# Performance work log

Measured on AMD Instinct MI355X. Metric: run time of the kernel, lower is better.

Reference implementation:

```python
import jax, jax.numpy as jnp
import numpy as np

TEMPERATURE = 0.07


def setup_inputs() -> dict:
    key = jax.random.key(0)
    k1, k2, k3 = jax.random.split(key, 3)
    B, D = 8192, 256
    projections = jax.random.normal(k1, (B, D), dtype=jnp.float32)
    affordance_ids = jax.random.randint(k2, (B,), 0, 16, dtype=jnp.int64)
    instance_ids = jax.random.randint(k3, (B,), 0, 4096, dtype=jnp.int64)
    return {
        "projections": projections,
        "affordance_ids": affordance_ids,
        "instance_ids": instance_ids,
    }


def reference(projections, affordance_ids, instance_ids):
    B = projections.shape[0]
    # (B, B) similarity logits
    sim = jnp.matmul(projections, projections.T) / TEMPERATURE
    aff_mask = affordance_ids[:, None] == affordance_ids[None, :]
    inst_mask = instance_ids[:, None] == instance_ids[None, :]
    positive_mask = aff_mask & (~inst_mask)
    self_mask = jnp.eye(B, dtype=bool)
    # per-row logsumexp over all j != i (stable, single pass)
    masked_sim = jnp.where(self_mask, -jnp.inf, sim)
    lse = jax.nn.logsumexp(masked_sim, axis=1)  # (B,)
    # loss per positive pair: -sim[i,j] + lse[i]
    per_pair = jnp.where(positive_mask, lse[:, None] - sim, 0.0)
    num_pairs = jnp.sum(positive_mask)
    total = jnp.sum(per_pair)
    return jnp.where(num_pairs > 0, total / num_pairs.astype(sim.dtype), 0.0)
```

## Files before the change

kernel.cpp:

```cpp
#include <hip/hip_runtime.h>
#include <hip/hip_bf16.h>
#include <stdint.h>

#define BN 8192
#define DK 256
#define KLOG2E_T 20.609929155556617f
#define INV_T 14.285714285714286f
#define NEGINF (-3.0e38f)

typedef short vshort8 __attribute__((ext_vector_type(8)));
typedef float vfloat16 __attribute__((ext_vector_type(16)));

__device__ __forceinline__ void gload16(const void* g, void* lds) {
  __builtin_amdgcn_global_load_lds(
      (const __attribute__((address_space(1))) unsigned int*)g,
      (__attribute__((address_space(3))) unsigned int*)lds, 16, 0, 0);
}

__global__ __launch_bounds__(256) void prep_g(
    const float* __restrict__ P, const int* __restrict__ aff,
    const int* __restrict__ inst, ushort* __restrict__ Pb,
    int* __restrict__ keys, int* __restrict__ head, int* __restrict__ nxt,
    int* __restrict__ cntA, float* __restrict__ G) {
  __shared__ float4 Gl[4][16][64];
  __shared__ int hist[16];
  const int t = threadIdx.x;
  const int rg = t >> 6, c = t & 63;
  for (int idx = t; idx < 4096; idx += 256)
    ((float4*)Gl)[idx] = make_float4(0.f, 0.f, 0.f, 0.f);
  if (t < 16) hist[t] = 0;
  __syncthreads();
  const int r0 = blockIdx.x * 64;
  for (int k = 0; k < 16; ++k) {
    const int r = r0 + k * 4 + rg;
    float4 v = ((const float4*)(P + (size_t)r * DK))[c];
    ushort4 h;
    __hip_bfloat16 b;
    b = __float2bfloat16(v.x); h.x = __builtin_bit_cast(unsigned short, b);
    b = __float2bfloat16(v.y); h.y = __builtin_bit_cast(unsigned short, b);
    b = __float2bfloat16(v.z); h.z = __builtin_bit_cast(unsigned short, b);
    b = __float2bfloat16(v.w); h.w = __builtin_bit_cast(unsigned short, b);
    ((ushort4*)(Pb + (size_t)r * DK))[c] = h;
    const int a = aff[r];
    float4 g = Gl[rg][a][c];
    g.x += v.x; g.y += v.y; g.z += v.z; g.w += v.w;
    Gl[rg][a][c] = g;
  }
  if (t < 64) {
    const int g = r0 + t;
    const int a = aff[g];
    const int k = (a << 12) | inst[g];
    keys[g] = k;
    nxt[g] = atomicExch(&head[k], g + 1);
    atomicAdd(&hist[a], 1);
  }
  __syncthreads();
  if (t < 16) atomicAdd(&cntA[t], hist[t]);
  for (int idx = t; idx < 1024; idx += 256) {
    const int a = idx >> 6, cc = idx & 63;
    float4 s0 = Gl[0][a][cc], s1 = Gl[1][a][cc];
    float4 s2 = Gl[2][a][cc], s3 = Gl[3][a][cc];
    atomicAdd(&G[a * 256 + cc * 4 + 0], s0.x + s1.x + s2.x + s3.x);
    atomicAdd(&G[a * 256 + cc * 4 + 1], s0.y + s1.y + s2.y + s3.y);
    atomicAdd(&G[a * 256 + cc * 4 + 2], s0.z + s1.z + s2.z + s3.z);
    atomicAdd(&G[a * 256 + cc * 4 + 3], s0.w + s1.w + s2.w + s3.w);
  }
}

__global__ __launch_bounds__(512, 2) void fused_kernel(
    const ushort* __restrict__ Pb, float2* __restrict__ stats) {
  __shared__ __align__(16) char AbufB[8 * 128 * 64];
  __shared__ __align__(16) char BbufB[2 * 512 * 64];
  __shared__ float2 red[8][2][32];

  const int tid = threadIdx.x;
  const int w = tid >> 6;
  const int l = tid & 63;
  const int lo = l & 31;
  const int hi = l >> 5;
  const int iw = w >> 2;
  const int jw = w & 3;

  const int bid = blockIdx.x;
  const int xcd = bid & 7;
  const int local = bid >> 3;
  const int jc = (xcd << 1) | (local & 1);
  const int it = local >> 1;
  const int ibase = it * 128;
  const int jcbase = jc * 512;

  const int srow = tid >> 2;
  const int sswz = ((tid & 3) ^ ((srow >> 1) & 3)) * 16;
  const char* gA = (const char*)(Pb + (size_t)ibase * DK);
  const char* gB = (const char*)(Pb + (size_t)jcbase * DK);

#pragma unroll
  for (int e = 0; e < 8; ++e)
    gload16(gA + (size_t)srow * 512 + e * 64 + sswz, AbufB + e * 8192 + tid * 16);
#pragma unroll
  for (int e = 0; e < 4; ++e)
    gload16(gB + (size_t)(e * 128 + srow) * 512 + sswz,
            BbufB + e * 8192 + tid * 16);
  __syncthreads();

  const int rowa = iw * 64 + lo;
  const int rowb = jw * 128 + lo;
  const int rsw = (lo >> 1) & 3;
  const int sw0 = ((0 + hi) ^ rsw) * 16;
  const int sw1 = ((2 + hi) ^ rsw) * 16;

  vfloat16 acc[2][4];
#pragma unroll
  for (int mi = 0; mi < 2; ++mi)
#pragma unroll
    for (int nj = 0; nj < 4; ++nj)
#pragma unroll
      for (int r = 0; r < 16; ++r) acc[mi][nj][r] = 0.f;

  for (int kc = 0; kc < 8; ++kc) {
    if (kc < 7) {
      char* dst = BbufB + ((kc + 1) & 1) * 32768 + tid * 16;
      const char* src = gB + (size_t)srow * 512 + (kc + 1) * 64 + sswz;
#pragma unroll
      for (int e = 0; e < 4; ++e)
        gload16(src + (size_t)e * 128 * 512, dst + e * 8192);
    }
    const char* As = AbufB + kc * 8192;
    const char* Bs = BbufB + (kc & 1) * 32768;
#pragma unroll
    for (int kk = 0; kk < 2; ++kk) {
      const int so = kk ? sw1 : sw0;
      vshort8 a0 = *(const vshort8*)(As + rowa * 64 + so);
      vshort8 a1 = *(const vshort8*)(As + (rowa + 32) * 64 + so);
#pragma unroll
      for (int nj = 0; nj < 4; ++nj) {
        vshort8 jf = *(const vshort8*)(Bs + (rowb + nj * 32) * 64 + so);
        acc[0][nj] = __builtin_amdgcn_mfma_f32_32x32x16_bf16(jf, a0, acc[0][nj], 0, 0, 0);
        acc[1][nj] = __builtin_amdgcn_mfma_f32_32x32x16_bf16(jf, a1, acc[1][nj], 0, 0, 0);
      }
    }
    __syncthreads();
  }

  float mx[2] = {NEGINF, NEGINF};
#pragma unroll
  for (int mi = 0; mi < 2; ++mi) {
    const int gib = ibase + iw * 64 + mi * 32;
#pragma unroll
    for (int nj = 0; nj < 4; ++nj) {
      const bool dia = gib == (jcbase + jw * 128 + nj * 32);
      if (dia) {
#pragma unroll
        for (int r = 0; r < 16; ++r) {
          const int jj = (r & 3) + 8 * (r >> 2) + 4 * hi;
          if (jj == lo) acc[mi][nj][r] = NEGINF;
        }
      }
#pragma unroll
      for (int r = 0; r < 16; ++r) mx[mi] = fmaxf(mx[mi], acc[mi][nj][r]);
    }
  }
  mx[0] = fmaxf(mx[0], __shfl_xor(mx[0], 32));
  mx[1] = fmaxf(mx[1], __shfl_xor(mx[1], 32));
  float s[2] = {0.f, 0.f};
#pragma unroll
  for (int mi = 0; mi < 2; ++mi) {
    const float rc = -mx[mi] * KLOG2E_T;
#pragma unroll
    for (int nj = 0; nj < 4; ++nj)
#pragma unroll
      for (int r = 0; r < 16; ++r)
        s[mi] += exp2f(fmaf(acc[mi][nj][r], KLOG2E_T, rc));
  }
  s[0] += __shfl_xor(s[0], 32);
  s[1] += __shfl_xor(s[1], 32);
  if (l < 32) {
    red[w][0][lo] = make_float2(mx[0], s[0]);
    red[w][1][lo] = make_float2(mx[1], s[1]);
  }
  __syncthreads();
  if (tid < 128) {
    const int iw2 = tid >> 6, mi2 = (tid >> 5) & 1, lo2 = tid & 31;
    float2 a = red[iw2 * 4 + 0][mi2][lo2];
    float mm = a.x, ss = a.y;
#pragma unroll
    for (int j2 = 1; j2 < 4; ++j2) {
      float2 b = red[iw2 * 4 + j2][mi2][lo2];
      float M = fmaxf(mm, b.x);
      ss = ss * exp2f((mm - M) * KLOG2E_T) + b.y * exp2f((b.x - M) * KLOG2E_T);
      mm = M;
    }
    stats[(size_t)jc * BN + ibase + iw2 * 64 + mi2 * 32 + lo2] = make_float2(mm, ss);
  }
}

__global__ __launch_bounds__(256) void final_rows(
    const float2* __restrict__ stats, const float* __restrict__ P,
    const float* __restrict__ G, const int* __restrict__ keys,
    const int* __restrict__ head, const int* __restrict__ nxt,
    const int* __restrict__ cntA, float2* __restrict__ part) {
  const int t = threadIdx.x;
  const int rloc = t >> 6;
  const int lane = t & 63;
  const int i = blockIdx.x * 4 + rloc;

  float2 st = stats[(size_t)(lane & 15) * BN + i];
  float mm = st.x, ss = st.y;
#pragma unroll
  for (int off = 1; off < 16; off <<= 1) {
    float mo = __shfl_xor(mm, off);
    float so = __shfl_xor(ss, off);
    float M = fmaxf(mm, mo);
    ss = ss * exp2f((mm - M) * KLOG2E_T) + so * exp2f((mo - M) * KLOG2E_T);
    mm = M;
  }
  const float lse = logf(ss) + mm * INV_T;

  const int key = keys[i];
  const int a = key >> 12;
  float4 p4 = ((const float4*)(P + (size_t)i * 256))[lane];
  float4 g4 = ((const float4*)(G + a * 256))[lane];
  float acc = p4.x * g4.x + p4.y * g4.y + p4.z * g4.z + p4.w * g4.w;
  int cnt = 0;
  int j = head[key];
  while (j > 0) {
    const int jr = j - 1;
    float4 q4 = ((const float4*)(P + (size_t)jr * 256))[lane];
    acc -= p4.x * q4.x + p4.y * q4.y + p4.z * q4.z + p4.w * q4.w;
    cnt++;
    j = nxt[jr];
  }
#pragma unroll
  for (int off = 1; off < 64; off <<= 1) acc += __shfl_xor(acc, off);
  const float pc = (float)(cntA[a] - cnt);
  const float contrib = pc * lse - acc * INV_T;

  __shared__ float cs[4], ps[4];
  if (lane == 0) { cs[rloc] = contrib; ps[rloc] = pc; }
  __syncthreads();
  if (t == 0)
    part[blockIdx.x] = make_float2(cs[0] + cs[1] + cs[2] + cs[3],
                                   ps[0] + ps[1] + ps[2] + ps[3]);
}

__global__ void finalize(const float2* __restrict__ part, float* __restrict__ out) {
  const int t = threadIdx.x;
  float c = 0.f, p = 0.f;
  for (int k = t; k < 2048; k += 256) {
    float2 v = part[k];
    c += v.x;
    p += v.y;
  }
#pragma unroll
  for (int off = 1; off < 64; off <<= 1) {
    c += __shfl_xor(c, off);
    p += __shfl_xor(p, off);
  }
  __shared__ float cs[4], ps[4];
  if ((t & 63) == 0) { cs[t >> 6] = c; ps[t >> 6] = p; }
  __syncthreads();
  if (t == 0) {
    c = cs[0] + cs[1] + cs[2] + cs[3];
    p = ps[0] + ps[1] + ps[2] + ps[3];
    out[0] = (p > 0.f) ? (c / p) : 0.f;
  }
}

extern "C" void kernel_launch(void* const* d_in, const int* in_sizes, int n_in,
                              void* d_out, int out_size, void* d_ws, size_t ws_size,
                              hipStream_t stream) {
  const float* P = (const float*)d_in[0];
  const int* aff = (const int*)d_in[1];
  const int* inst = (const int*)d_in[2];
  char* ws = (char*)d_ws;
  ushort* Pb    = (ushort*)(ws);
  int*    keys  = (int*)(ws + 4194304);
  int*    nxt   = (int*)(ws + 4227072);
  int*    head  = (int*)(ws + 4259840);
  float*  G     = (float*)(ws + 4521984);
  int*    cntA  = (int*)(ws + 4538368);
  float2* stats = (float2*)(ws + 4538496);
  float2* part  = (float2*)(ws + 5587072);
  float* out = (float*)d_out;

  hipMemsetAsync(head, 0, 278592, stream);
  prep_g<<<128, 256, 0, stream>>>(P, aff, inst, Pb, keys, head, nxt, cntA, G);
  fused_kernel<<<1024, 512, 0, stream>>>(Pb, stats);
  final_rows<<<2048, 256, 0, stream>>>(stats, P, G, keys, head, nxt, cntA, part);
  finalize<<<1, 256, 0, stream>>>(part, out);
}
```

Before: 91.98 us.

## Retile fused Gram kernel to 256x256 blocks with 4-wave 128x128 warp tiles

The fused similarity kernel moves from a 128x512 block tile with 8 waves of 64x128 to a 256x256 block tile with 4 waves, each computing 128x128 (4x4 MFMA tiles). A and B are both streamed in 128-byte K slices with double buffering and an 8-way XOR swizzle, where before all of A was resident. The column-chunk count doubles to 32, so the stats buffer grows and final_rows merges 32 partial max/sum pairs per row. The aim is higher MFMA-to-LDS-read reuse per wave, at the cost of more accumulator registers (256 floats per lane), lower occupancy, and a deeper final merge.

Result: slower. 99.70 us (+8.4%).

```diff
diff --git a/kernel.cpp b/kernel.cpp
--- a/kernel.cpp
+++ b/kernel.cpp
@@ -67,131 +67,128 @@
   }
 }
 
-__global__ __launch_bounds__(512, 2) void fused_kernel(
+__global__ __launch_bounds__(256, 1) void fused_kernel(
     const ushort* __restrict__ Pb, float2* __restrict__ stats) {
-  __shared__ __align__(16) char AbufB[8 * 128 * 64];
-  __shared__ __align__(16) char BbufB[2 * 512 * 64];
-  __shared__ float2 red[8][2][32];
+  __shared__ __align__(16) char Ab[2][32768];
+  __shared__ __align__(16) char Bb[2][32768];
+  __shared__ float2 red[2][256];
 
   const int tid = threadIdx.x;
   const int w = tid >> 6;
   const int l = tid & 63;
   const int lo = l & 31;
   const int hi = l >> 5;
-  const int iw = w >> 2;
-  const int jw = w & 3;
+  const int iw = w >> 1;
+  const int jw = w & 1;
 
   const int bid = blockIdx.x;
   const int xcd = bid & 7;
-  const int local = bid >> 3;
-  const int jc = (xcd << 1) | (local & 1);
-  const int it = local >> 1;
-  const int ibase = it * 128;
-  const int jcbase = jc * 512;
-
-  const int srow = tid >> 2;
-  const int sswz = ((tid & 3) ^ ((srow >> 1) & 3)) * 16;
+  const int inner = (bid >> 3) & 3;
+  const int it = bid >> 5;
+  const int jc = xcd * 4 + inner;
+  const int ibase = it * 256;
+  const int jcbase = jc * 256;
+
+  const int trow = tid >> 3;
+  const int sswz = ((tid & 7) ^ (trow & 7)) * 16;
   const char* gA = (const char*)(Pb + (size_t)ibase * DK);
   const char* gB = (const char*)(Pb + (size_t)jcbase * DK);
 
-#pragma unroll
-  for (int e = 0; e < 8; ++e)
-    gload16(gA + (size_t)srow * 512 + e * 64 + sswz, AbufB + e * 8192 + tid * 16);
-#pragma unroll
-  for (int e = 0; e < 4; ++e)
-    gload16(gB + (size_t)(e * 128 + srow) * 512 + sswz,
-            BbufB + e * 8192 + tid * 16);
-  __syncthreads();
-
-  const int rowa = iw * 64 + lo;
-  const int rowb = jw * 128 + lo;
-  const int rsw = (lo >> 1) & 3;
-  const int sw0 = ((0 + hi) ^ rsw) * 16;
-  const int sw1 = ((2 + hi) ^ rsw) * 16;
-
-  vfloat16 acc[2][4];
-#pragma unroll
-  for (int mi = 0; mi < 2; ++mi)
+#define STAGE(ks, bsel)                                                        \
+  {                                                                            \
+    const int ko = (ks) * 128;                                                 \
+    _Pragma("unroll") for (int e = 0; e < 8; ++e) {                            \
+      gload16(gA + (size_t)(trow + 32 * e) * 512 + ko + sswz,                  \
+              Ab[bsel] + e * 4096 + tid * 16);                                 \
+      gload16(gB + (size_t)(trow + 32 * e) * 512 + ko + sswz,                  \
+              Bb[bsel] + e * 4096 + tid * 16);                                 \
+    }                                                                          \
+  }
+
+  STAGE(0, 0);
+
+  vfloat16 acc[4][4];
+#pragma unroll
+  for (int mi = 0; mi < 4; ++mi)
 #pragma unroll
     for (int nj = 0; nj < 4; ++nj)
 #pragma unroll
       for (int r = 0; r < 16; ++r) acc[mi][nj][r] = 0.f;
 
-  for (int kc = 0; kc < 8; ++kc) {
-    if (kc < 7) {
-      char* dst = BbufB + ((kc + 1) & 1) * 32768 + tid * 16;
-      const char* src = gB + (size_t)srow * 512 + (kc + 1) * 64 + sswz;
-#pragma unroll
-      for (int e = 0; e < 4; ++e)
-        gload16(src + (size_t)e * 128 * 512, dst + e * 8192);
-    }
-    const char* As = AbufB + kc * 8192;
-    const char* Bs = BbufB + (kc & 1) * 32768;
-#pragma unroll
-    for (int kk = 0; kk < 2; ++kk) {
-      const int so = kk ? sw1 : sw0;
-      vshort8 a0 = *(const vshort8*)(As + rowa * 64 + so);
-      vshort8 a1 = *(const vshort8*)(As + (rowa + 32) * 64 + so);
-#pragma unroll
-      for (int nj = 0; nj < 4; ++nj) {
-        vshort8 jf = *(const vshort8*)(Bs + (rowb + nj * 32) * 64 + so);
-        acc[0][nj] = __builtin_amdgcn_mfma_f32_32x32x16_bf16(jf, a0, acc[0][nj], 0, 0, 0);
-        acc[1][nj] = __builtin_amdgcn_mfma_f32_32x32x16_bf16(jf, a1, acc[1][nj], 0, 0, 0);
+  const int rAb = iw * 128 + lo;
+  const int rBb = jw * 128 + lo;
+
+  __syncthreads();
+
+  for (int ks = 0; ks < 4; ++ks) {
+    if (ks < 3) STAGE(ks + 1, (ks + 1) & 1);
+    const char* As = Ab[ks & 1];
+    const char* Bs = Bb[ks & 1];
+#pragma unroll
+    for (int kk = 0; kk < 4; ++kk) {
+      const int so = ((kk * 2 + hi) ^ (lo & 7)) * 16;
+      vshort8 af0 = *(const vshort8*)(As + (rAb + 0) * 128 + so);
+      vshort8 af1 = *(const vshort8*)(As + (rAb + 32) * 128 + so);
+      vshort8 af2 = *(const vshort8*)(As + (rAb + 64) * 128 + so);
+      vshort8 af3 = *(const vshort8*)(As + (rAb + 96) * 128 + so);
+      vshort8 bf0 = *(const vshort8*)(Bs + (rBb + 0) * 128 + so);
+      vshort8 bf1 = *(const vshort8*)(Bs + (rBb + 32) * 128 + so);
+      vshort8 bf2 = *(const vshort8*)(Bs + (rBb + 64) * 128 + so);
+      vshort8 bf3 = *(const vshort8*)(Bs + (rBb + 96) * 128 + so);
+#pragma unroll
+      for (int mi = 0; mi < 4; ++mi) {
+        vshort8 af = mi == 0 ? af0 : mi == 1 ? af1 : mi == 2 ? af2 : af3;
+        acc[mi][0] = __builtin_amdgcn_mfma_f32_32x32x16_bf16(bf0, af, acc[mi][0], 0, 0, 0);
+        acc[mi][1] = __builtin_amdgcn_mfma_f32_32x32x16_bf16(bf1, af, acc[mi][1], 0, 0, 0);
+        acc[mi][2] = __builtin_amdgcn_mfma_f32_32x32x16_bf16(bf2, af, acc[mi][2], 0, 0, 0);
+        acc[mi][3] = __builtin_amdgcn_mfma_f32_32x32x16_bf16(bf3, af, acc[mi][3], 0, 0, 0);
       }
     }
     __syncthreads();
   }
 
-  float mx[2] = {NEGINF, NEGINF};
-#pragma unroll
-  for (int mi = 0; mi < 2; ++mi) {
-    const int gib = ibase + iw * 64 + mi * 32;
+#pragma unroll
+  for (int mi = 0; mi < 4; ++mi) {
+    const int gib = ibase + iw * 128 + mi * 32;
 #pragma unroll
     for (int nj = 0; nj < 4; ++nj) {
-      const bool dia = gib == (jcbase + jw * 128 + nj * 32);
-      if (dia) {
+      if (gib == (jcbase + jw * 128 + nj * 32)) {
 #pragma unroll
         for (int r = 0; r < 16; ++r) {
           const int jj = (r & 3) + 8 * (r >> 2) + 4 * hi;
           if (jj == lo) acc[mi][nj][r] = NEGINF;
         }
       }
-#pragma unroll
-      for (int r = 0; r < 16; ++r) mx[mi] = fmaxf(mx[mi], acc[mi][nj][r]);
     }
   }
-  mx[0] = fmaxf(mx[0], __shfl_xor(mx[0], 32));
-  mx[1] = fmaxf(mx[1], __shfl_xor(mx[1], 32));
-  float s[2] = {0.f, 0.f};
-#pragma unroll
-  for (int mi = 0; mi < 2; ++mi) {
-    const float rc = -mx[mi] * KLOG2E_T;
+#pragma unroll
+  for (int mi = 0; mi < 4; ++mi) {
+    float mx = NEGINF;
 #pragma unroll
     for (int nj = 0; nj < 4; ++nj)
 #pragma unroll
+      for (int r = 0; r < 16; ++r) mx = fmaxf(mx, acc[mi][nj][r]);
+    mx = fmaxf(mx, __shfl_xor(mx, 32));
+    const float rc = -mx * KLOG2E_T;
+    float sv = 0.f;
+#pragma unroll
+    for (int nj = 0; nj < 4; ++nj)
+#pragma unroll
       for (int r = 0; r < 16; ++r)
-        s[mi] += exp2f(fmaf(acc[mi][nj][r], KLOG2E_T, rc));
-  }
-  s[0] += __shfl_xor(s[0], 32);
-  s[1] += __shfl_xor(s[1], 32);
-  if (l < 32) {
-    red[w][0][lo] = make_float2(mx[0], s[0]);
-    red[w][1][lo] = make_float2(mx[1], s[1]);
-  }
-  __syncthreads();
-  if (tid < 128) {
-    const int iw2 = tid >> 6, mi2 = (tid >> 5) & 1, lo2 = tid & 31;
-    float2 a = red[iw2 * 4 + 0][mi2][lo2];
-    float mm = a.x, ss = a.y;
-#pragma unroll
-    for (int j2 = 1; j2 < 4; ++j2) {
-      float2 b = red[iw2 * 4 + j2][mi2][lo2];
-      float M = fmaxf(mm, b.x);
-      ss = ss * exp2f((mm - M) * KLOG2E_T) + b.y * exp2f((b.x - M) * KLOG2E_T);
-      mm = M;
-    }
-    stats[(size_t)jc * BN + ibase + iw2 * 64 + mi2 * 32 + lo2] = make_float2(mm, ss);
-  }
+        sv += exp2f(fmaf(acc[mi][nj][r], KLOG2E_T, rc));
+    sv += __shfl_xor(sv, 32);
+    if (hi == 0) red[jw][iw * 128 + mi * 32 + lo] = make_float2(mx, sv);
+  }
+  __syncthreads();
+  {
+    const float2 a = red[0][tid];
+    const float2 b = red[1][tid];
+    const float M = fmaxf(a.x, b.x);
+    const float ss = a.y * exp2f((a.x - M) * KLOG2E_T) +
+                     b.y * exp2f((b.x - M) * KLOG2E_T);
+    stats[(size_t)jc * BN + ibase + tid] = make_float2(M, ss);
+  }
+#undef STAGE
 }
 
 __global__ __launch_bounds__(256) void final_rows(
@@ -204,10 +201,10 @@
   const int lane = t & 63;
   const int i = blockIdx.x * 4 + rloc;
 
-  float2 st = stats[(size_t)(lane & 15) * BN + i];
+  float2 st = stats[(size_t)(lane & 31) * BN + i];
   float mm = st.x, ss = st.y;
 #pragma unroll
-  for (int off = 1; off < 16; off <<= 1) {
+  for (int off = 1; off < 32; off <<= 1) {
     float mo = __shfl_xor(mm, off);
     float so = __shfl_xor(ss, off);
     float M = fmaxf(mm, mo);
@@ -280,12 +277,12 @@
   float*  G     = (float*)(ws + 4521984);
   int*    cntA  = (int*)(ws + 4538368);
   float2* stats = (float2*)(ws + 4538496);
-  float2* part  = (float2*)(ws + 5587072);
+  float2* part  = (float2*)(ws + 6635648);
   float* out = (float*)d_out;
 
   hipMemsetAsync(head, 0, 278592, stream);
   prep_g<<<128, 256, 0, stream>>>(P, aff, inst, Pb, keys, head, nxt, cntA, G);
-  fused_kernel<<<1024, 512, 0, stream>>>(Pb, stats);
+  fused_kernel<<<1024, 256, 0, stream>>>(Pb, stats);
   final_rows<<<2048, 256, 0, stream>>>(stats, P, G, keys, head, nxt, cntA, part);
   finalize<<<1, 256, 0, stream>>>(part, out);
 }
```
